# Kernel optimization log

Hardware: AMD Instinct MI355X
Metric: run time of the kernel (lower is better)

The kernel has to match this reference:

```python
import jax, jax.numpy as jnp
import numpy as np

# ---- static config (from init_kwargs) ----
B_, L_, DM = 4, 2048, 1024
EXPAND, HEADDIM, DSTATE, DCONV = 2, 64, 64, 7
DIN = EXPAND * DM            # 2048
NH = DIN // HEADDIM          # 32
CONV_DIM = DIN + 2 * DSTATE  # 2176 (x, B, C go through the depthwise conv)
DPROJ = 2 * DIN + 2 * DSTATE + 2 * NH  # 4288 (z, xBC, dt_fwd, dt_bwd)
EPS = 1e-5


def setup_inputs() -> dict:
    key = jax.random.key(0)
    ks = jax.random.split(key, 8)
    s = lambda d: 1.0 / np.sqrt(d)
    # dt_bias = inv_softplus(dt) with dt ~ logUniform(1e-3, 0.1)  (Mamba2/Hydra init)
    dt = jnp.exp(jax.random.uniform(ks[3], (NH,)) * (np.log(0.1) - np.log(0.001)) + np.log(0.001))
    return {
        "x": jax.random.normal(ks[0], (B_, L_, DM), jnp.float32),
        "ln_gamma": jnp.ones((DM,), jnp.float32),
        "ln_beta": jnp.zeros((DM,), jnp.float32),
        "W_in": jax.random.normal(ks[1], (DPROJ, DM), jnp.float32) * s(DM),
        "conv_w": jax.random.normal(ks[2], (CONV_DIM, DCONV), jnp.float32) * s(DCONV),
        "conv_b": jnp.zeros((CONV_DIM,), jnp.float32),
        "dt_bias": jnp.log(jnp.expm1(dt)),
        "A_log": jnp.log(jax.random.uniform(ks[4], (NH,), minval=1.0, maxval=16.0)),
        "fc_D_w": jax.random.normal(ks[5], (NH, DIN), jnp.float32) * s(DIN),
        "D": jnp.ones((NH,), jnp.float32),
        "norm_w": jnp.ones((DIN,), jnp.float32),
        "W_out": jax.random.normal(ks[6], (DM, DIN), jnp.float32) * s(DIN),
    }


def _hydra_layer(x, ln_gamma, ln_beta, W_in, conv_w, conv_b, dt_bias, A_log,
                 fc_D_w, D, norm_w, W_out):
    res = x
    # LayerNorm
    mu = jnp.mean(x, -1, keepdims=True)
    var = jnp.mean((x - mu) ** 2, -1, keepdims=True)
    u = (x - mu) * jax.lax.rsqrt(var + EPS) * ln_gamma + ln_beta

    # input projection -> z (gate), xBC (conv stream), dt (fwd+bwd)
    zxbcdt = jnp.einsum('bld,pd->blp', u, W_in)
    z = zxbcdt[..., :DIN]
    xBC = zxbcdt[..., DIN:DIN + CONV_DIM]
    dt = zxbcdt[..., DIN + CONV_DIM:]               # (B,L,2*NH)

    # depthwise 'same' conv along L + SiLU (bidirectional model -> symmetric pad)
    xBC_c = jax.lax.conv_general_dilated(
        xBC.transpose(0, 2, 1), conv_w[:, None, :], (1,),
        [(DCONV // 2, DCONV // 2)], feature_group_count=CONV_DIM)
    xBC = jax.nn.silu((xBC_c + conv_b[None, :, None]).transpose(0, 2, 1))

    xs = xBC[..., :DIN]                             # (B,L,DIN)
    Bm = xBC[..., DIN:DIN + DSTATE]                 # (B,L,N)
    Cm = xBC[..., DIN + DSTATE:]                    # (B,L,N)

    flip = lambda a: a[:, ::-1]
    # stack forward and (flipped) backward direction along batch
    dt2 = jax.nn.softplus(jnp.concatenate([dt[..., :NH], flip(dt[..., NH:])], 0) + dt_bias)  # (2B,L,NH)
    x2 = jnp.concatenate([xs, flip(xs)], 0).reshape(2 * B_, L_, NH, HEADDIM)
    B2 = jnp.concatenate([Bm, flip(Bm)], 0)
    C2 = jnp.concatenate([Cm, flip(Cm)], 0)

    A = -jnp.exp(A_log)                             # (NH,)
    dA = jnp.exp(dt2 * A)                           # (2B,L,NH)

    # selective SSM recurrence: h_t = dA_t * h_{t-1} + dt_t * x_t B_t^T ; y_t = h_t C_t
    def step(h, inp):
        dA_t, dt_t, B_t, C_t, x_t = inp
        dBx = (dt_t[:, :, None, None] * x_t[..., None]) * B_t[:, None, None, :]
        h = dA_t[:, :, None, None] * h + dBx        # (2B,NH,P,N)
        y = jnp.einsum('bhpn,bn->bhp', h, C_t)
        return h, y

    h0 = jnp.zeros((2 * B_, NH, HEADDIM, DSTATE), x.dtype)
    tr = lambda a: jnp.moveaxis(a, 1, 0)
    _, ys = jax.lax.scan(step, h0, (tr(dA), tr(dt2), tr(B2), tr(C2), tr(x2)))
    y = jnp.moveaxis(ys, 0, 1)                      # (2B,L,NH,P)

    # shift by one: strictly off-diagonal part of the quasiseparable mixing matrix
    y = jnp.concatenate([jnp.zeros_like(y[:, :1]), y[:, :-1]], axis=1)
    y = y[:B_] + flip(y[B_:])                       # (B,L,NH,P)

    # data-dependent diagonal: D(x) = fc_D(x) + D, applied per head
    Ddata = jnp.einsum('bld,hd->blh', xs, fc_D_w) + D
    y = y + xs.reshape(B_, L_, NH, HEADDIM) * Ddata[..., None]
    y = y.reshape(B_, L_, DIN)

    # gated RMSNorm (norm after gate)
    y = y * jax.nn.silu(z)
    y = y * jax.lax.rsqrt(jnp.mean(y * y, -1, keepdims=True) + EPS) * norm_w

    # out proj + residual (dropout is identity in eval)
    return res + jnp.einsum('bli,di->bld', y, W_out)


def reference(x, ln_gamma, ln_beta, W_in, conv_w, conv_b, dt_bias, A_log,
              fc_D_w, D, norm_w, W_out):
    return _hydra_layer(x, ln_gamma, ln_beta, W_in, conv_w, conv_b, dt_bias,
                        A_log, fc_D_w, D, norm_w, W_out)
```

## Files before the change

### kernel.cpp

```cpp
#include <hip/hip_runtime.h>
#include <stdint.h>

#define B_   4
#define L_   2048
#define DM   1024
#define DIN  2048
#define NH   32
#define HD   64
#define DSTATE 64
#define DCONV  7
#define CONV_DIM 2176
#define DPROJ 4288
#define NPAD 4352
#define BL   8192
#define EPS  1e-5f
#define QC   128
#define NCH  16

typedef unsigned short u16;
typedef unsigned int   u32;
typedef __bf16 bf16x8 __attribute__((ext_vector_type(8)));
typedef float  f32x4  __attribute__((ext_vector_type(4)));

__device__ __forceinline__ float b2f(u32 b) { return __uint_as_float(b << 16); }
__device__ __forceinline__ u16 f2b(float f) {
    u32 u = __float_as_uint(f);
    u32 r = (u + 0x7fffu + ((u >> 16) & 1u)) >> 16;
    return (u16)r;
}
__device__ __forceinline__ void unpack8(uint4 v, float* f) {
    f[0] = b2f(v.x & 0xffffu); f[1] = b2f(v.x >> 16);
    f[2] = b2f(v.y & 0xffffu); f[3] = b2f(v.y >> 16);
    f[4] = b2f(v.z & 0xffffu); f[5] = b2f(v.z >> 16);
    f[6] = b2f(v.w & 0xffffu); f[7] = b2f(v.w >> 16);
}
__device__ __forceinline__ uint4 pack8(const float* f) {
    uint4 v;
    v.x = (u32)f2b(f[0]) | ((u32)f2b(f[1]) << 16);
    v.y = (u32)f2b(f[2]) | ((u32)f2b(f[3]) << 16);
    v.z = (u32)f2b(f[4]) | ((u32)f2b(f[5]) << 16);
    v.w = (u32)f2b(f[6]) | ((u32)f2b(f[7]) << 16);
    return v;
}
__device__ __forceinline__ void gload_lds16(const u16* g, u16* l) {
    __builtin_amdgcn_global_load_lds((const __attribute__((address_space(1))) void*)g,
                                     (__attribute__((address_space(3))) void*)l, 16, 0, 0);
}

__global__ __launch_bounds__(256) void k_cvt_win(const float* __restrict__ W, u16* __restrict__ Wb) {
    int idx = blockIdx.x * 256 + threadIdx.x;
    int n = idx >> 10;
    float v = (n < DPROJ) ? W[(size_t)n * DM + (idx & 1023)] : 0.f;
    Wb[idx] = f2b(v);
}
__global__ __launch_bounds__(256) void k_cvt_wout(const float* __restrict__ W, u16* __restrict__ Wb) {
    int idx = blockIdx.x * 256 + threadIdx.x;
    Wb[idx] = f2b(W[idx]);
}
__global__ __launch_bounds__(256) void k_cvt_fcd(const float* __restrict__ W, u16* __restrict__ Wb) {
    int idx = blockIdx.x * 256 + threadIdx.x;
    Wb[idx] = f2b(W[idx]);
}

__global__ __launch_bounds__(256) void k_ln(const float* __restrict__ x, const float* __restrict__ g,
                                            const float* __restrict__ be, u16* __restrict__ u) {
    int row = blockIdx.x, tid = threadIdx.x;
    const float4* xr = (const float4*)(x + (size_t)row * DM);
    float4 v = xr[tid];
    float s1 = v.x + v.y + v.z + v.w;
    float s2 = v.x * v.x + v.y * v.y + v.z * v.z + v.w * v.w;
    for (int o = 32; o; o >>= 1) { s1 += __shfl_down(s1, o); s2 += __shfl_down(s2, o); }
    __shared__ float ls1[4], ls2[4];
    int w = tid >> 6;
    if ((tid & 63) == 0) { ls1[w] = s1; ls2[w] = s2; }
    __syncthreads();
    float t1 = ls1[0] + ls1[1] + ls1[2] + ls1[3];
    float t2 = ls2[0] + ls2[1] + ls2[2] + ls2[3];
    float mu = t1 * (1.f / DM);
    float var = t2 * (1.f / DM) - mu * mu;
    float rs = rsqrtf(var + EPS);
    float4 gv = ((const float4*)g)[tid];
    float4 bv = ((const float4*)be)[tid];
    float o0 = (v.x - mu) * rs * gv.x + bv.x;
    float o1 = (v.y - mu) * rs * gv.y + bv.y;
    float o2 = (v.z - mu) * rs * gv.z + bv.z;
    float o3 = (v.w - mu) * rs * gv.w + bv.w;
    uint2 p;
    p.x = (u32)f2b(o0) | ((u32)f2b(o1) << 16);
    p.y = (u32)f2b(o2) | ((u32)f2b(o3) << 16);
    ((uint2*)(u + (size_t)row * DM))[tid] = p;
}

__global__ __launch_bounds__(256) void k_gemm_bt(const u16* __restrict__ A, const u16* __restrict__ Bw,
                                                 int M, int N, int K, int out_bf16,
                                                 u16* __restrict__ obf, int ldo,
                                                 float* __restrict__ ofp, const float* __restrict__ res) {
    __shared__ __align__(16) u16 As[128 * 32];
    __shared__ __align__(16) u16 Bs[128 * 32];
    int tid = threadIdx.x;
    int m0 = blockIdx.y * 128, n0 = blockIdx.x * 128;
    int w = tid >> 6, lane = tid & 63;
    int wm = (w >> 1) * 64, wn = (w & 1) * 64;
    int lr = lane & 15, lq = lane >> 4;
    int r = (tid >> 2), kc = tid & 3;

    f32x4 acc[4][4];
    #pragma unroll
    for (int i = 0; i < 4; i++)
        #pragma unroll
        for (int j = 0; j < 4; j++) acc[i][j] = (f32x4){0.f, 0.f, 0.f, 0.f};

    for (int kt = 0; kt < K; kt += 32) {
        #pragma unroll
        for (int it = 0; it < 2; it++) {
            u16* lbase_a = &As[(it * 256 + w * 64) * 8];
            u16* lbase_b = &Bs[(it * 256 + w * 64) * 8];
            int rr = r + it * 64;
            gload_lds16(A + (size_t)(m0 + rr) * K + kt + kc * 8, lbase_a);
            gload_lds16(Bw + (size_t)(n0 + rr) * K + kt + kc * 8, lbase_b);
        }
        __syncthreads();
        bf16x8 af[4], bfr[4];
        #pragma unroll
        for (int i = 0; i < 4; i++) af[i] = *(const bf16x8*)&As[(wm + 16 * i + lr) * 32 + lq * 8];
        #pragma unroll
        for (int j = 0; j < 4; j++) bfr[j] = *(const bf16x8*)&Bs[(wn + 16 * j + lr) * 32 + lq * 8];
        #pragma unroll
        for (int i = 0; i < 4; i++)
            #pragma unroll
            for (int j = 0; j < 4; j++)
                acc[i][j] = __builtin_amdgcn_mfma_f32_16x16x32_bf16(af[i], bfr[j], acc[i][j], 0, 0, 0);
        __syncthreads();
    }
    #pragma unroll
    for (int i = 0; i < 4; i++) {
        #pragma unroll
        for (int j = 0; j < 4; j++) {
            #pragma unroll
            for (int rr = 0; rr < 4; rr++) {
                int m = m0 + wm + 16 * i + lq * 4 + rr;
                int n = n0 + wn + 16 * j + lr;
                float v = acc[i][j][rr];
                if (out_bf16) obf[(size_t)m * ldo + n] = f2b(v);
                else          ofp[(size_t)m * ldo + n] = v + res[(size_t)m * ldo + n];
            }
        }
    }
}

__global__ __launch_bounds__(256) void k_dproj(const u16* __restrict__ xs, const u16* __restrict__ fcb,
                                               const float* __restrict__ Dv, float* __restrict__ Dd) {
    __shared__ __align__(16) u16 As[32 * 64];
    __shared__ __align__(16) u16 Bs[32 * 64];
    int tid = threadIdx.x;
    int m0 = blockIdx.x * 32;
    int w = tid >> 6, lane = tid & 63, lr = lane & 15, lq = lane >> 4;
    int mt = (w & 1) * 16, nt = (w >> 1) * 16;
    int r = tid >> 3, kc = tid & 7;
    f32x4 acc = (f32x4){0.f, 0.f, 0.f, 0.f};
    for (int kt = 0; kt < DIN; kt += 64) {
        ((uint4*)As)[tid] = *(const uint4*)(xs + (size_t)(m0 + r) * DIN + kt + kc * 8);
        ((uint4*)Bs)[tid] = *(const uint4*)(fcb + (size_t)r * DIN + kt + kc * 8);
        __syncthreads();
        #pragma unroll
        for (int ks = 0; ks < 2; ks++) {
            bf16x8 a = *(const bf16x8*)&As[(mt + lr) * 64 + ks * 32 + lq * 8];
            bf16x8 b = *(const bf16x8*)&Bs[(nt + lr) * 64 + ks * 32 + lq * 8];
            acc = __builtin_amdgcn_mfma_f32_16x16x32_bf16(a, b, acc, 0, 0, 0);
        }
        __syncthreads();
    }
    #pragma unroll
    for (int rr = 0; rr < 4; rr++) {
        int m = m0 + mt + lq * 4 + rr;
        int n = nt + lr;
        Dd[(size_t)m * 32 + n] = acc[rr] + Dv[n];
    }
}

__global__ __launch_bounds__(256) void k_conv(const u16* __restrict__ zx, const float* __restrict__ cw,
                                              const float* __restrict__ cb, u16* __restrict__ xs,
                                              float* __restrict__ BC) {
    __shared__ u16 sh[262 * 64];
    int c0 = blockIdx.x * 64, t0 = blockIdx.y * 256, b = blockIdx.z;
    int tid = threadIdx.x;
    int c = tid & 63, tg = tid >> 6;
    for (int it = 0; it < 66; it++) {
        int r = it * 4 + tg;
        if (r < 262) {
            int t = t0 + r - 3;
            u16 v = 0;
            if (t >= 0 && t < L_) v = zx[(size_t)(b * L_ + t) * NPAD + DIN + c0 + c];
            sh[r * 64 + c] = v;
        }
    }
    float wgt[7];
    #pragma unroll
    for (int k = 0; k < 7; k++) wgt[k] = cw[(c0 + c) * 7 + k];
    float bias = cb[c0 + c];
    __syncthreads();
    int cg = c0 + c;
    for (int tt = 0; tt < 64; tt++) {
        int tl = tt * 4 + tg;
        float a = bias;
        #pragma unroll
        for (int k = 0; k < 7; k++) a += b2f(sh[(tl + k) * 64 + c]) * wgt[k];
        float v = a / (1.f + __expf(-a));
        size_t row = (size_t)b * L_ + (t0 + tl);
        if (cg < DIN) xs[row * DIN + cg] = f2b(v);
        else          BC[row * 128 + (cg - DIN)] = v;
    }
}

__global__ __launch_bounds__(256) void k_dt(const u16* __restrict__ zx, const float* __restrict__ dt_bias,
                                            const float* __restrict__ A_log, float* __restrict__ dtA) {
    int idx = blockIdx.x * 256 + threadIdx.x;
    int row = idx >> 6, j = idx & 63;
    float draw = b2f(zx[(size_t)row * NPAD + (DIN + CONV_DIM) + j]);
    float xb = draw + dt_bias[j & 31];
    float dt2 = (xb > 20.f) ? xb : log1pf(__expf(xb));
    dtA[(size_t)idx * 2]     = dt2;
    dtA[(size_t)idx * 2 + 1] = -__expf(A_log[j & 31]) * dt2;
}

__global__ __launch_bounds__(256) void k_chunk(const u16* __restrict__ xs, const float* __restrict__ BC,
                                               const float* __restrict__ dtA, u16* __restrict__ y0,
                                               u16* __restrict__ y1, float* __restrict__ wout,
                                               float* __restrict__ decay) {
    __shared__ __align__(16) u16 ab[18432];
    __shared__ __align__(16) u16 XT[64 * 136];
    __shared__ __align__(16) float dts_s[128];
    __shared__ __align__(16) float lda_s[128];
    __shared__ __align__(16) double cumd[128];

    const int blk = blockIdx.x;
    const int c = blk & 15, dbh = blk >> 4;
    const int h = dbh & 31, b = (dbh >> 5) & 3, dir = dbh >> 7;
    const int tid = threadIdx.x, w = tid >> 6, lane = tid & 63, lr = lane & 15, lq = lane >> 4;
    const int s0 = c * QC;
    u16* yo = dir ? y1 : y0;

    if (tid < 128) {
        int s = s0 + tid;
        int t = dir ? (L_ - 1 - s) : s;
        size_t di = ((size_t)(b * L_ + t) * 64 + dir * 32 + h) * 2;
        dts_s[tid] = dtA[di];
        lda_s[tid] = dtA[di + 1];
    }
    {
        int sl0 = tid >> 3, ng = (tid & 7) * 8;
        #pragma unroll
        for (int it = 0; it < 4; it++) {
            int sl = sl0 + it * 32;
            int s = s0 + sl;
            int t = dir ? (L_ - 1 - s) : s;
            size_t row = (size_t)b * L_ + t;
            const float* bcr = BC + row * 128;
            float f[8];
            float4 v0 = *(const float4*)(bcr + 64 + ng);
            float4 v1 = *(const float4*)(bcr + 64 + ng + 4);
            f[0]=v0.x; f[1]=v0.y; f[2]=v0.z; f[3]=v0.w; f[4]=v1.x; f[5]=v1.y; f[6]=v1.z; f[7]=v1.w;
            *(uint4*)&ab[sl * 72 + ng] = pack8(f);
            v0 = *(const float4*)(bcr + ng);
            v1 = *(const float4*)(bcr + ng + 4);
            f[0]=v0.x; f[1]=v0.y; f[2]=v0.z; f[3]=v0.w; f[4]=v1.x; f[5]=v1.y; f[6]=v1.z; f[7]=v1.w;
            *(uint4*)&ab[9216 + sl * 72 + ng] = pack8(f);
            uint4 xv = *(const uint4*)(xs + row * DIN + h * 64 + ng);
            u16 xh[8] = {(u16)(xv.x & 0xffffu), (u16)(xv.x >> 16), (u16)(xv.y & 0xffffu), (u16)(xv.y >> 16),
                         (u16)(xv.z & 0xffffu), (u16)(xv.z >> 16), (u16)(xv.w & 0xffffu), (u16)(xv.w >> 16)};
            #pragma unroll
            for (int i = 0; i < 8; i++) XT[(ng + i) * 136 + sl] = xh[i];
        }
    }
    __syncthreads();
    if (w == 0) {
        double v0 = (double)lda_s[lane];
        double v1 = (double)lda_s[64 + lane];
        #pragma unroll
        for (int o = 1; o < 64; o <<= 1) {
            double t0 = __shfl_up(v0, o);
            double t1 = __shfl_up(v1, o);
            if (lane >= o) { v0 += t0; v1 += t1; }
        }
        double tot0 = __shfl(v0, 63);
        cumd[lane] = v0;
        cumd[64 + lane] = tot0 + v1;
    }
    bf16x8 af[2][2];
    #pragma unroll
    for (int ti = 0; ti < 2; ti++)
        #pragma unroll
        for (int ks = 0; ks < 2; ks++)
            af[ti][ks] = *(const bf16x8*)&ab[(w * 32 + ti * 16 + lr) * 72 + ks * 32 + lq * 8];
    f32x4 accg[2][8];
    #pragma unroll
    for (int ti = 0; ti < 2; ti++)
        #pragma unroll
        for (int si = 0; si < 8; si++) accg[ti][si] = (f32x4){0.f, 0.f, 0.f, 0.f};
    #pragma unroll
    for (int si = 0; si < 8; si++)
        #pragma unroll
        for (int ks = 0; ks < 2; ks++) {
            bf16x8 bf = *(const bf16x8*)&ab[9216 + (si * 16 + lr) * 72 + ks * 32 + lq * 8];
            accg[0][si] = __builtin_amdgcn_mfma_f32_16x16x32_bf16(af[0][ks], bf, accg[0][si], 0, 0, 0);
            accg[1][si] = __builtin_amdgcn_mfma_f32_16x16x32_bf16(af[1][ks], bf, accg[1][si], 0, 0, 0);
        }
    __syncthreads();
    {
        double cumt_d[8];
        #pragma unroll
        for (int ti = 0; ti < 2; ti++)
            #pragma unroll
            for (int r = 0; r < 4; r++) cumt_d[ti * 4 + r] = cumd[w * 32 + ti * 16 + lq * 4 + r];
        double cums_d[8]; float dts_l[8];
        #pragma unroll
        for (int si = 0; si < 8; si++) { cums_d[si] = cumd[si * 16 + lr]; dts_l[si] = dts_s[si * 16 + lr]; }
        #pragma unroll
        for (int ti = 0; ti < 2; ti++)
            #pragma unroll
            for (int si = 0; si < 8; si++)
                #pragma unroll
                for (int r = 0; r < 4; r++) {
                    int t_l = w * 32 + ti * 16 + lq * 4 + r;
                    int s_l = si * 16 + lr;
                    float v = 0.f;
                    if (s_l <= t_l)
                        v = __expf((float)(cumt_d[ti * 4 + r] - cums_d[si])) * dts_l[si] * accg[ti][si][r];
                    ab[t_l * 136 + s_l] = f2b(v);
                }
    }
    __syncthreads();
    f32x4 acc[2][4];
    #pragma unroll
    for (int ti = 0; ti < 2; ti++)
        #pragma unroll
        for (int pj = 0; pj < 4; pj++) acc[ti][pj] = (f32x4){0.f, 0.f, 0.f, 0.f};
    #pragma unroll
    for (int ks = 0; ks < 4; ks++) {
        bf16x8 a0 = *(const bf16x8*)&ab[(w * 32 + lr) * 136 + ks * 32 + lq * 8];
        bf16x8 a1 = *(const bf16x8*)&ab[(w * 32 + 16 + lr) * 136 + ks * 32 + lq * 8];
        #pragma unroll
        for (int pj = 0; pj < 4; pj++) {
            bf16x8 bf = *(const bf16x8*)&XT[(pj * 16 + lr) * 136 + ks * 32 + lq * 8];
            acc[0][pj] = __builtin_amdgcn_mfma_f32_16x16x32_bf16(a0, bf, acc[0][pj], 0, 0, 0);
            acc[1][pj] = __builtin_amdgcn_mfma_f32_16x16x32_bf16(a1, bf, acc[1][pj], 0, 0, 0);
        }
    }
    #pragma unroll
    for (int ti = 0; ti < 2; ti++)
        #pragma unroll
        for (int pj = 0; pj < 4; pj++)
            #pragma unroll
            for (int r = 0; r < 4; r++) {
                int t_l = w * 32 + ti * 16 + lq * 4 + r;
                int s = s0 + t_l;
                int t = dir ? (L_ - 1 - s) : s;
                yo[((size_t)b * L_ + t) * DIN + h * 64 + pj * 16 + lr] = f2b(acc[ti][pj][r]);
            }
    if (tid < 128) wout[dbh * 2048 + s0 + tid] = __expf((float)cumd[tid]);
    if (tid == 0)  decay[blk] = __expf((float)cumd[127]);
}

__global__ __launch_bounds__(256) void k_state(const u16* __restrict__ xs, const float* __restrict__ BC,
                                               const float* __restrict__ dtA, u16* __restrict__ scb) {
    __shared__ __align__(16) u16 XT[64 * 136];
    __shared__ __align__(16) u16 BT[64 * 136];
    __shared__ __align__(16) float dts_s[128];
    __shared__ __align__(16) float lda_s[128];
    __shared__ __align__(16) float wend[128];

    const int blk = blockIdx.x;
    const int c = blk & 15, dbh = blk >> 4;
    const int h = dbh & 31, b = (dbh >> 5) & 3, dir = dbh >> 7;
    const int tid = threadIdx.x, w = tid >> 6, lane = tid & 63, lr = lane & 15, lq = lane >> 4;
    const int s0 = c * QC;

    if (tid < 128) {
        int s = s0 + tid;
        int t = dir ? (L_ - 1 - s) : s;
        size_t di = ((size_t)(b * L_ + t) * 64 + dir * 32 + h) * 2;
        dts_s[tid] = dtA[di];
        lda_s[tid] = dtA[di + 1];
    }
    {
        int sl0 = tid >> 3, ng = (tid & 7) * 8;
        #pragma unroll
        for (int it = 0; it < 4; it++) {
            int sl = sl0 + it * 32;
            int s = s0 + sl;
            int t = dir ? (L_ - 1 - s) : s;
            size_t row = (size_t)b * L_ + t;
            const float* bcr = BC + row * 128;
            float4 v0 = *(const float4*)(bcr + ng);
            float4 v1 = *(const float4*)(bcr + ng + 4);
            float f[8] = {v0.x, v0.y, v0.z, v0.w, v1.x, v1.y, v1.z, v1.w};
            #pragma unroll
            for (int i = 0; i < 8; i++) BT[(ng + i) * 136 + sl] = f2b(f[i]);
            uint4 xv = *(const uint4*)(xs + row * DIN + h * 64 + ng);
            u16 xh[8] = {(u16)(xv.x & 0xffffu), (u16)(xv.x >> 16), (u16)(xv.y & 0xffffu), (u16)(xv.y >> 16),
                         (u16)(xv.z & 0xffffu), (u16)(xv.z >> 16), (u16)(xv.w & 0xffffu), (u16)(xv.w >> 16)};
            #pragma unroll
            for (int i = 0; i < 8; i++) XT[(ng + i) * 136 + sl] = xh[i];
        }
    }
    __syncthreads();
    if (w == 0) {
        double v0 = (double)lda_s[lane];
        double v1 = (double)lda_s[64 + lane];
        #pragma unroll
        for (int o = 1; o < 64; o <<= 1) {
            double t0 = __shfl_up(v0, o);
            double t1 = __shfl_up(v1, o);
            if (lane >= o) { v0 += t0; v1 += t1; }
        }
        double tot0 = __shfl(v0, 63);
        double tot  = tot0 + __shfl(v1, 63);
        wend[lane]      = __expf((float)(tot - v0)) * dts_s[lane];
        wend[64 + lane] = __expf((float)(tot - (tot0 + v1))) * dts_s[64 + lane];
    }
    __syncthreads();
    f32x4 acc[4];
    #pragma unroll
    for (int nj = 0; nj < 4; nj++) acc[nj] = (f32x4){0.f, 0.f, 0.f, 0.f};
    #pragma unroll
    for (int ks = 0; ks < 4; ks++) {
        uint4 xv = *(const uint4*)&XT[(w * 16 + lr) * 136 + ks * 32 + lq * 8];
        float xf[8]; unpack8(xv, xf);
        float4 w0 = *(const float4*)&wend[ks * 32 + lq * 8];
        float4 w1 = *(const float4*)&wend[ks * 32 + lq * 8 + 4];
        float fs[8] = {xf[0]*w0.x, xf[1]*w0.y, xf[2]*w0.z, xf[3]*w0.w,
                       xf[4]*w1.x, xf[5]*w1.y, xf[6]*w1.z, xf[7]*w1.w};
        bf16x8 a = __builtin_bit_cast(bf16x8, pack8(fs));
        #pragma unroll
        for (int nj = 0; nj < 4; nj++) {
            bf16x8 bb = *(const bf16x8*)&BT[(nj * 16 + lr) * 136 + ks * 32 + lq * 8];
            acc[nj] = __builtin_amdgcn_mfma_f32_16x16x32_bf16(a, bb, acc[nj], 0, 0, 0);
        }
    }
    #pragma unroll
    for (int nj = 0; nj < 4; nj++)
        #pragma unroll
        for (int r = 0; r < 4; r++) {
            int p = w * 16 + lq * 4 + r, n = nj * 16 + lr;
            scb[(size_t)blk * 4096 + p * 64 + n] = f2b(acc[nj][r]);
        }
}

__global__ __launch_bounds__(256) void k_carry(const float* __restrict__ BC, const float* __restrict__ wout,
                                               const float* __restrict__ decay, const u16* __restrict__ scb,
                                               u16* __restrict__ y0, u16* __restrict__ y1) {
    __shared__ __align__(16) float hsh[64 * 68];
    __shared__ __align__(16) u16 Csc[128 * 72];
    __shared__ __align__(16) u16 ybs[128 * 72];
    __shared__ __align__(16) u16 prevu[72];
    const int dbh = blockIdx.x;
    const int h = dbh & 31, b = (dbh >> 5) & 3, dir = dbh >> 7;
    const int tid = threadIdx.x, w = tid >> 6, lane = tid & 63, lr = lane & 15, lq = lane >> 4;
    u16* yo = dir ? y1 : y0;

    for (int i = tid; i < 64 * 68; i += 256) hsh[i] = 0.f;
    if (tid < 72) prevu[tid] = 0;
    __syncthreads();
    const int sl0 = tid >> 3, ng = (tid & 7) * 8;
    for (int c = 0; c < NCH; c++) {
        #pragma unroll
        for (int it = 0; it < 4; it++) {
            int sl = sl0 + it * 32;
            int s = c * QC + sl;
            int t = dir ? (L_ - 1 - s) : s;
            const float* bcr = BC + ((size_t)b * L_ + t) * 128 + 64 + ng;
            float sc = wout[dbh * 2048 + s];
            float4 v0 = *(const float4*)bcr;
            float4 v1 = *(const float4*)(bcr + 4);
            float f[8] = {v0.x*sc, v0.y*sc, v0.z*sc, v0.w*sc, v1.x*sc, v1.y*sc, v1.z*sc, v1.w*sc};
            *(uint4*)&Csc[sl * 72 + ng] = pack8(f);
        }
        bf16x8 hb[4][2];
        #pragma unroll
        for (int pj = 0; pj < 4; pj++)
            #pragma unroll
            for (int ks = 0; ks < 2; ks++) {
                const float* hp = &hsh[(pj * 16 + lr) * 68 + ks * 32 + lq * 8];
                float4 a0 = *(const float4*)hp;
                float4 a1 = *(const float4*)(hp + 4);
                float f[8] = {a0.x, a0.y, a0.z, a0.w, a1.x, a1.y, a1.z, a1.w};
                hb[pj][ks] = __builtin_bit_cast(bf16x8, pack8(f));
            }
        __syncthreads();
        f32x4 acc[2][4];
        #pragma unroll
        for (int ti = 0; ti < 2; ti++)
            #pragma unroll
            for (int pj = 0; pj < 4; pj++) acc[ti][pj] = (f32x4){0.f, 0.f, 0.f, 0.f};
        #pragma unroll
        for (int ks = 0; ks < 2; ks++) {
            bf16x8 a0 = *(const bf16x8*)&Csc[(w * 32 + lr) * 72 + ks * 32 + lq * 8];
            bf16x8 a1 = *(const bf16x8*)&Csc[(w * 32 + 16 + lr) * 72 + ks * 32 + lq * 8];
            #pragma unroll
            for (int pj = 0; pj < 4; pj++) {
                acc[0][pj] = __builtin_amdgcn_mfma_f32_16x16x32_bf16(a0, hb[pj][ks], acc[0][pj], 0, 0, 0);
                acc[1][pj] = __builtin_amdgcn_mfma_f32_16x16x32_bf16(a1, hb[pj][ks], acc[1][pj], 0, 0, 0);
            }
        }
        #pragma unroll
        for (int ti = 0; ti < 2; ti++)
            #pragma unroll
            for (int pj = 0; pj < 4; pj++)
                #pragma unroll
                for (int r = 0; r < 4; r++) {
                    int t_l = w * 32 + ti * 16 + lq * 4 + r;
                    int s = c * QC + t_l;
                    int t = dir ? (L_ - 1 - s) : s;
                    float yv = acc[ti][pj][r] + b2f(yo[((size_t)b * L_ + t) * DIN + h * 64 + pj * 16 + lr]);
                    ybs[t_l * 72 + pj * 16 + lr] = f2b(yv);
                }
        {
            float dk = decay[dbh * 16 + c];
            const u16* sg = scb + ((size_t)(dbh * 16 + c)) * 4096 + tid * 16;
            uint4 q0 = *(const uint4*)sg;
            uint4 q1 = *(const uint4*)(sg + 8);
            float sf[16]; unpack8(q0, sf); unpack8(q1, sf + 8);
            int p = (tid * 16) >> 6, n0 = (tid * 16) & 63;
            float* hp = &hsh[p * 68 + n0];
            #pragma unroll
            for (int i = 0; i < 16; i++) hp[i] = dk * hp[i] + sf[i];
        }
        __syncthreads();
        #pragma unroll
        for (int it = 0; it < 4; it++) {
            int sl = sl0 + it * 32;
            int s = c * QC + sl;
            int t = dir ? (L_ - 1 - s) : s;
            const u16* src = (sl == 0) ? (prevu + ng) : &ybs[(sl - 1) * 72 + ng];
            *(uint4*)&yo[((size_t)b * L_ + t) * DIN + h * 64 + ng] = *(const uint4*)src;
        }
        __syncthreads();
        if (tid < 8) *(uint4*)&prevu[tid * 8] = *(const uint4*)&ybs[127 * 72 + tid * 8];
    }
}

__global__ __launch_bounds__(256) void k_gate(const u16* __restrict__ xs, const u16* __restrict__ zx,
                                              const u16* __restrict__ y0, const u16* __restrict__ y1,
                                              const float* __restrict__ Dd,
                                              const float* __restrict__ nw, u16* __restrict__ yn) {
    int row = blockIdx.x, tid = threadIdx.x;
    __shared__ float red[4];
    size_t base = (size_t)row * DIN;
    uint4 xv = ((const uint4*)(xs + base))[tid];
    uint4 zv = ((const uint4*)(zx + (size_t)row * NPAD))[tid];
    uint4 a0 = ((const uint4*)(y0 + base))[tid];
    uint4 a1 = ((const uint4*)(y1 + base))[tid];
    float sD = Dd[(size_t)row * 32 + (tid >> 3)];
    float xf[8], zf[8], f0[8], f1[8];
    unpack8(xv, xf); unpack8(zv, zf); unpack8(a0, f0); unpack8(a1, f1);
    int d0 = tid * 8;
    float g[8]; float ss = 0.f;
    #pragma unroll
    for (int i = 0; i < 8; i++) {
        float yv = f0[i] + f1[i] + xf[i] * sD;
        float z = zf[i];
        float gg = yv * (z / (1.f + __expf(-z)));
        g[i] = gg; ss += gg * gg;
    }
    for (int o = 32; o; o >>= 1) ss += __shfl_down(ss, o);
    if ((tid & 63) == 0) red[tid >> 6] = ss;
    __syncthreads();
    float tot = red[0] + red[1] + red[2] + red[3];
    float r = rsqrtf(tot * (1.f / DIN) + EPS);
    float o8[8];
    #pragma unroll
    for (int i = 0; i < 8; i++) o8[i] = g[i] * r * nw[d0 + i];
    ((uint4*)(yn + base))[tid] = pack8(o8);
}

#define OFF_U     ((size_t)0)
#define OFF_WIN   ((size_t)16777216)
#define OFF_WOUT  ((size_t)25690112)
#define OFF_ZX    ((size_t)29884416)
#define OFF_XS    ((size_t)101187584)
#define OFF_BC    ((size_t)134742016)
#define OFF_DTA   ((size_t)138936320)
#define OFF_Y0    ((size_t)143130624)
#define OFF_Y1    ((size_t)176685056)
#define OFF_YN    ((size_t)210239488)
#define OFF_WO2   OFF_U
#define OFF_DEC   (OFF_U + 2097152)
#define OFF_FCB   (OFF_U + 2113536)
#define OFF_DD    (OFF_U + 2244608)
#define OFF_SCB   OFF_YN

extern "C" void kernel_launch(void* const* d_in, const int* in_sizes, int n_in,
                              void* d_out, int out_size, void* d_ws, size_t ws_size,
                              hipStream_t stream) {
    const float* x       = (const float*)d_in[0];
    const float* ln_g    = (const float*)d_in[1];
    const float* ln_b    = (const float*)d_in[2];
    const float* W_in    = (const float*)d_in[3];
    const float* conv_w  = (const float*)d_in[4];
    const float* conv_b  = (const float*)d_in[5];
    const float* dt_bias = (const float*)d_in[6];
    const float* A_log   = (const float*)d_in[7];
    const float* fc_D_w  = (const float*)d_in[8];
    const float* Dv      = (const float*)d_in[9];
    const float* norm_w  = (const float*)d_in[10];
    const float* W_out   = (const float*)d_in[11];

    char* ws = (char*)d_ws;
    u16*   u_bf  = (u16*)(ws + OFF_U);
    u16*   winb  = (u16*)(ws + OFF_WIN);
    u16*   woutb = (u16*)(ws + OFF_WOUT);
    u16*   zx    = (u16*)(ws + OFF_ZX);
    u16*   xs    = (u16*)(ws + OFF_XS);
    float* BC    = (float*)(ws + OFF_BC);
    float* dtA   = (float*)(ws + OFF_DTA);
    u16*   y0b   = (u16*)(ws + OFF_Y0);
    u16*   y1b   = (u16*)(ws + OFF_Y1);
    u16*   ynb   = (u16*)(ws + OFF_YN);
    float* wo2   = (float*)(ws + OFF_WO2);
    float* dec   = (float*)(ws + OFF_DEC);
    u16*   fcb   = (u16*)(ws + OFF_FCB);
    float* Dd    = (float*)(ws + OFF_DD);
    u16*   scb   = (u16*)(ws + OFF_SCB);

    k_cvt_win <<<(NPAD * DM) / 256, 256, 0, stream>>>(W_in, winb);
    k_cvt_wout<<<(DM * DIN) / 256, 256, 0, stream>>>(W_out, woutb);
    k_ln      <<<BL, 256, 0, stream>>>(x, ln_g, ln_b, u_bf);
    k_gemm_bt <<<dim3(NPAD / 128, BL / 128), 256, 0, stream>>>(u_bf, winb, BL, NPAD, DM, 1, zx, NPAD, nullptr, nullptr);
    k_cvt_fcd <<<(NH * DIN) / 256, 256, 0, stream>>>(fc_D_w, fcb);
    k_conv    <<<dim3(CONV_DIM / 64, L_ / 256, B_), 256, 0, stream>>>(zx, conv_w, conv_b, xs, BC);
    k_dt      <<<(BL * 64) / 256, 256, 0, stream>>>(zx, dt_bias, A_log, dtA);
    k_dproj   <<<BL / 32, 256, 0, stream>>>(xs, fcb, Dv, Dd);
    k_chunk   <<<4096, 256, 0, stream>>>(xs, BC, dtA, y0b, y1b, wo2, dec);
    k_state   <<<4096, 256, 0, stream>>>(xs, BC, dtA, scb);
    k_carry   <<<256, 256, 0, stream>>>(BC, wo2, dec, scb, y0b, y1b);
    k_gate    <<<BL, 256, 0, stream>>>(xs, zx, y0b, y1b, Dd, norm_w, ynb);
    k_gemm_bt <<<dim3(DM / 128, BL / 128), 256, 0, stream>>>(ynb, woutb, BL, DM, DIN, 0, nullptr, DM, (float*)d_out, x);
}
```

Before: 594.1 us.

## Fuse chunk-state kernel into k_chunk and swizzle GEMM LDS layout

Merges the separate k_state kernel into k_chunk so the chunk's B, x tiles and cumulative decay are loaded and computed once, removing a second pass over xs/BC/dtA and a launch. The tiled GEMM now XOR-swizzles the k-column group per row pair to cut LDS bank conflicts on fragment reads, and k_dproj pads its LDS rows to 72 for the same reason. In exchange k_chunk uses more shared memory (an extra transposed B tile and wend), which may lower its occupancy.

```diff
diff --git a/kernel.cpp b/kernel.cpp
--- a/kernel.cpp
+++ b/kernel.cpp
@@ -102,7 +102,6 @@
     int w = tid >> 6, lane = tid & 63;
     int wm = (w >> 1) * 64, wn = (w & 1) * 64;
     int lr = lane & 15, lq = lane >> 4;
-    int r = (tid >> 2), kc = tid & 3;
 
     f32x4 acc[4][4];
     #pragma unroll
@@ -113,18 +112,26 @@
     for (int kt = 0; kt < K; kt += 32) {
         #pragma unroll
         for (int it = 0; it < 2; it++) {
+            int s_idx = it * 256 + tid;
+            int row = s_idx >> 2;
+            int kcg = (s_idx & 3) ^ ((row >> 1) & 3);
             u16* lbase_a = &As[(it * 256 + w * 64) * 8];
             u16* lbase_b = &Bs[(it * 256 + w * 64) * 8];
-            int rr = r + it * 64;
-            gload_lds16(A + (size_t)(m0 + rr) * K + kt + kc * 8, lbase_a);
-            gload_lds16(Bw + (size_t)(n0 + rr) * K + kt + kc * 8, lbase_b);
+            gload_lds16(A + (size_t)(m0 + row) * K + kt + kcg * 8, lbase_a);
+            gload_lds16(Bw + (size_t)(n0 + row) * K + kt + kcg * 8, lbase_b);
         }
         __syncthreads();
         bf16x8 af[4], bfr[4];
         #pragma unroll
-        for (int i = 0; i < 4; i++) af[i] = *(const bf16x8*)&As[(wm + 16 * i + lr) * 32 + lq * 8];
-        #pragma unroll
-        for (int j = 0; j < 4; j++) bfr[j] = *(const bf16x8*)&Bs[(wn + 16 * j + lr) * 32 + lq * 8];
+        for (int i = 0; i < 4; i++) {
+            int row = wm + 16 * i + lr;
+            af[i] = *(const bf16x8*)&As[row * 32 + (lq ^ ((row >> 1) & 3)) * 8];
+        }
+        #pragma unroll
+        for (int j = 0; j < 4; j++) {
+            int row = wn + 16 * j + lr;
+            bfr[j] = *(const bf16x8*)&Bs[row * 32 + (lq ^ ((row >> 1) & 3)) * 8];
+        }
         #pragma unroll
         for (int i = 0; i < 4; i++)
             #pragma unroll
@@ -150,8 +157,8 @@
 
 __global__ __launch_bounds__(256) void k_dproj(const u16* __restrict__ xs, const u16* __restrict__ fcb,
                                                const float* __restrict__ Dv, float* __restrict__ Dd) {
-    __shared__ __align__(16) u16 As[32 * 64];
-    __shared__ __align__(16) u16 Bs[32 * 64];
+    __shared__ __align__(16) u16 As[32 * 72];
+    __shared__ __align__(16) u16 Bs[32 * 72];
     int tid = threadIdx.x;
     int m0 = blockIdx.x * 32;
     int w = tid >> 6, lane = tid & 63, lr = lane & 15, lq = lane >> 4;
@@ -159,13 +166,13 @@
     int r = tid >> 3, kc = tid & 7;
     f32x4 acc = (f32x4){0.f, 0.f, 0.f, 0.f};
     for (int kt = 0; kt < DIN; kt += 64) {
-        ((uint4*)As)[tid] = *(const uint4*)(xs + (size_t)(m0 + r) * DIN + kt + kc * 8);
-        ((uint4*)Bs)[tid] = *(const uint4*)(fcb + (size_t)r * DIN + kt + kc * 8);
+        *(uint4*)&As[r * 72 + kc * 8] = *(const uint4*)(xs + (size_t)(m0 + r) * DIN + kt + kc * 8);
+        *(uint4*)&Bs[r * 72 + kc * 8] = *(const uint4*)(fcb + (size_t)r * DIN + kt + kc * 8);
         __syncthreads();
         #pragma unroll
         for (int ks = 0; ks < 2; ks++) {
-            bf16x8 a = *(const bf16x8*)&As[(mt + lr) * 64 + ks * 32 + lq * 8];
-            bf16x8 b = *(const bf16x8*)&Bs[(nt + lr) * 64 + ks * 32 + lq * 8];
+            bf16x8 a = *(const bf16x8*)&As[(mt + lr) * 72 + ks * 32 + lq * 8];
+            bf16x8 b = *(const bf16x8*)&Bs[(nt + lr) * 72 + ks * 32 + lq * 8];
             acc = __builtin_amdgcn_mfma_f32_16x16x32_bf16(a, b, acc, 0, 0, 0);
         }
         __syncthreads();
@@ -226,11 +233,13 @@
 __global__ __launch_bounds__(256) void k_chunk(const u16* __restrict__ xs, const float* __restrict__ BC,
                                                const float* __restrict__ dtA, u16* __restrict__ y0,
                                                u16* __restrict__ y1, float* __restrict__ wout,
-                                               float* __restrict__ decay) {
+                                               float* __restrict__ decay, u16* __restrict__ scb) {
     __shared__ __align__(16) u16 ab[18432];
     __shared__ __align__(16) u16 XT[64 * 136];
+    __shared__ __align__(16) u16 BT[64 * 136];
     __shared__ __align__(16) float dts_s[128];
     __shared__ __align__(16) float lda_s[128];
+    __shared__ __align__(16) float wend[128];
     __shared__ __align__(16) double cumd[128];
 
     const int blk = blockIdx.x;
@@ -264,7 +273,12 @@
             v0 = *(const float4*)(bcr + ng);
             v1 = *(const float4*)(bcr + ng + 4);
             f[0]=v0.x; f[1]=v0.y; f[2]=v0.z; f[3]=v0.w; f[4]=v1.x; f[5]=v1.y; f[6]=v1.z; f[7]=v1.w;
-            *(uint4*)&ab[9216 + sl * 72 + ng] = pack8(f);
+            uint4 pb = pack8(f);
+            *(uint4*)&ab[9216 + sl * 72 + ng] = pb;
+            u16 bh[8] = {(u16)(pb.x & 0xffffu), (u16)(pb.x >> 16), (u16)(pb.y & 0xffffu), (u16)(pb.y >> 16),
+                         (u16)(pb.z & 0xffffu), (u16)(pb.z >> 16), (u16)(pb.w & 0xffffu), (u16)(pb.w >> 16)};
+            #pragma unroll
+            for (int i = 0; i < 8; i++) BT[(ng + i) * 136 + sl] = bh[i];
             uint4 xv = *(const uint4*)(xs + row * DIN + h * 64 + ng);
             u16 xh[8] = {(u16)(xv.x & 0xffffu), (u16)(xv.x >> 16), (u16)(xv.y & 0xffffu), (u16)(xv.y >> 16),
                          (u16)(xv.z & 0xffffu), (u16)(xv.z >> 16), (u16)(xv.w & 0xffffu), (u16)(xv.w >> 16)};
@@ -306,6 +320,7 @@
             accg[1][si] = __builtin_amdgcn_mfma_f32_16x16x32_bf16(af[1][ks], bf, accg[1][si], 0, 0, 0);
         }
     __syncthreads();
+    if (tid < 128) wend[tid] = __expf((float)(cumd[127] - cumd[tid])) * dts_s[tid];
     {
         double cumt_d[8];
         #pragma unroll
@@ -357,71 +372,9 @@
                 int t = dir ? (L_ - 1 - s) : s;
                 yo[((size_t)b * L_ + t) * DIN + h * 64 + pj * 16 + lr] = f2b(acc[ti][pj][r]);
             }
-    if (tid < 128) wout[dbh * 2048 + s0 + tid] = __expf((float)cumd[tid]);
-    if (tid == 0)  decay[blk] = __expf((float)cumd[127]);
-}
-
-__global__ __launch_bounds__(256) void k_state(const u16* __restrict__ xs, const float* __restrict__ BC,
-                                               const float* __restrict__ dtA, u16* __restrict__ scb) {
-    __shared__ __align__(16) u16 XT[64 * 136];
-    __shared__ __align__(16) u16 BT[64 * 136];
-    __shared__ __align__(16) float dts_s[128];
-    __shared__ __align__(16) float lda_s[128];
-    __shared__ __align__(16) float wend[128];
-
-    const int blk = blockIdx.x;
-    const int c = blk & 15, dbh = blk >> 4;
-    const int h = dbh & 31, b = (dbh >> 5) & 3, dir = dbh >> 7;
-    const int tid = threadIdx.x, w = tid >> 6, lane = tid & 63, lr = lane & 15, lq = lane >> 4;
-    const int s0 = c * QC;
-
-    if (tid < 128) {
-        int s = s0 + tid;
-        int t = dir ? (L_ - 1 - s) : s;
-        size_t di = ((size_t)(b * L_ + t) * 64 + dir * 32 + h) * 2;
-        dts_s[tid] = dtA[di];
-        lda_s[tid] = dtA[di + 1];
-    }
-    {
-        int sl0 = tid >> 3, ng = (tid & 7) * 8;
-        #pragma unroll
-        for (int it = 0; it < 4; it++) {
-            int sl = sl0 + it * 32;
-            int s = s0 + sl;
-            int t = dir ? (L_ - 1 - s) : s;
-            size_t row = (size_t)b * L_ + t;
-            const float* bcr = BC + row * 128;
-            float4 v0 = *(const float4*)(bcr + ng);
-            float4 v1 = *(const float4*)(bcr + ng + 4);
-            float f[8] = {v0.x, v0.y, v0.z, v0.w, v1.x, v1.y, v1.z, v1.w};
-            #pragma unroll
-            for (int i = 0; i < 8; i++) BT[(ng + i) * 136 + sl] = f2b(f[i]);
-            uint4 xv = *(const uint4*)(xs + row * DIN + h * 64 + ng);
-            u16 xh[8] = {(u16)(xv.x & 0xffffu), (u16)(xv.x >> 16), (u16)(xv.y & 0xffffu), (u16)(xv.y >> 16),
-                         (u16)(xv.z & 0xffffu), (u16)(xv.z >> 16), (u16)(xv.w & 0xffffu), (u16)(xv.w >> 16)};
-            #pragma unroll
-            for (int i = 0; i < 8; i++) XT[(ng + i) * 136 + sl] = xh[i];
-        }
-    }
-    __syncthreads();
-    if (w == 0) {
-        double v0 = (double)lda_s[lane];
-        double v1 = (double)lda_s[64 + lane];
-        #pragma unroll
-        for (int o = 1; o < 64; o <<= 1) {
-            double t0 = __shfl_up(v0, o);
-            double t1 = __shfl_up(v1, o);
-            if (lane >= o) { v0 += t0; v1 += t1; }
-        }
-        double tot0 = __shfl(v0, 63);
-        double tot  = tot0 + __shfl(v1, 63);
-        wend[lane]      = __expf((float)(tot - v0)) * dts_s[lane];
-        wend[64 + lane] = __expf((float)(tot - (tot0 + v1))) * dts_s[64 + lane];
-    }
-    __syncthreads();
-    f32x4 acc[4];
-    #pragma unroll
-    for (int nj = 0; nj < 4; nj++) acc[nj] = (f32x4){0.f, 0.f, 0.f, 0.f};
+    f32x4 accs[4];
+    #pragma unroll
+    for (int nj = 0; nj < 4; nj++) accs[nj] = (f32x4){0.f, 0.f, 0.f, 0.f};
     #pragma unroll
     for (int ks = 0; ks < 4; ks++) {
         uint4 xv = *(const uint4*)&XT[(w * 16 + lr) * 136 + ks * 32 + lq * 8];
@@ -434,7 +387,7 @@
         #pragma unroll
         for (int nj = 0; nj < 4; nj++) {
             bf16x8 bb = *(const bf16x8*)&BT[(nj * 16 + lr) * 136 + ks * 32 + lq * 8];
-            acc[nj] = __builtin_amdgcn_mfma_f32_16x16x32_bf16(a, bb, acc[nj], 0, 0, 0);
+            accs[nj] = __builtin_amdgcn_mfma_f32_16x16x32_bf16(a, bb, accs[nj], 0, 0, 0);
         }
     }
     #pragma unroll
@@ -442,8 +395,10 @@
         #pragma unroll
         for (int r = 0; r < 4; r++) {
             int p = w * 16 + lq * 4 + r, n = nj * 16 + lr;
-            scb[(size_t)blk * 4096 + p * 64 + n] = f2b(acc[nj][r]);
-        }
+            scb[(size_t)blk * 4096 + p * 64 + n] = f2b(accs[nj][r]);
+        }
+    if (tid < 128) wout[dbh * 2048 + s0 + tid] = __expf((float)cumd[tid]);
+    if (tid == 0)  decay[blk] = __expf((float)cumd[127]);
 }
 
 __global__ __launch_bounds__(256) void k_carry(const float* __restrict__ BC, const float* __restrict__ wout,
@@ -630,8 +585,7 @@
     k_conv    <<<dim3(CONV_DIM / 64, L_ / 256, B_), 256, 0, stream>>>(zx, conv_w, conv_b, xs, BC);
     k_dt      <<<(BL * 64) / 256, 256, 0, stream>>>(zx, dt_bias, A_log, dtA);
     k_dproj   <<<BL / 32, 256, 0, stream>>>(xs, fcb, Dv, Dd);
-    k_chunk   <<<4096, 256, 0, stream>>>(xs, BC, dtA, y0b, y1b, wo2, dec);
-    k_state   <<<4096, 256, 0, stream>>>(xs, BC, dtA, scb);
+    k_chunk   <<<4096, 256, 0, stream>>>(xs, BC, dtA, y0b, y1b, wo2, dec, scb);
     k_carry   <<<256, 256, 0, stream>>>(BC, wo2, dec, scb, y0b, y1b);
     k_gate    <<<BL, 256, 0, stream>>>(xs, zx, y0b, y1b, Dd, norm_w, ynb);
     k_gemm_bt <<<dim3(DM / 128, BL / 128), 256, 0, stream>>>(ynb, woutb, BL, DM, DIN, 0, nullptr, DM, (float*)d_out, x);
```

Result: faster. 567.5 us (-4.5%).
